# Optimization experiments

Measured on AMD Instinct MI355X. Metric: run time of the kernel, lower is better.

Reference implementation:

```python
import jax, jax.numpy as jnp
import numpy as np

N_NODES = 100000
N_EDGES = 3200000
IN_DIM, HID_DIM, N_CLASS = 64, 32, 20


def setup_inputs() -> dict:
    key = jax.random.key(0)
    k1, k2, k3, k4, k5, k6 = jax.random.split(key, 6)
    x = jax.random.normal(k1, (N_NODES, IN_DIM), dtype=jnp.float32)
    edge_index = jax.random.randint(k2, (2, N_EDGES), 0, N_NODES, dtype=jnp.int64)
    W1 = jax.random.normal(k3, (IN_DIM, HID_DIM), dtype=jnp.float32) / np.sqrt(IN_DIM)
    b1 = jnp.zeros((HID_DIM,), dtype=jnp.float32)
    Wout = jax.random.normal(k4, (HID_DIM, N_CLASS), dtype=jnp.float32) / np.sqrt(HID_DIM)
    bout = jnp.zeros((N_CLASS,), dtype=jnp.float32)
    return {"x": x, "edge_index": edge_index, "W1": W1, "b1": b1, "Wout": Wout, "bout": bout}


def gcn_conv(x, edge_index, W, b):
    # PyG GCNConv defaults: add self-loops, symmetric deg^{-1/2} normalization.
    n = x.shape[0]
    loop = jnp.arange(n, dtype=edge_index.dtype)
    row = jnp.concatenate([edge_index[0], loop])  # source
    col = jnp.concatenate([edge_index[1], loop])  # target
    deg = jax.ops.segment_sum(jnp.ones_like(col, dtype=x.dtype), col, num_segments=n)
    dis = jnp.where(deg > 0, deg ** -0.5, 0.0)
    norm = dis[row] * dis[col]  # [E+N]
    xw = x @ W  # [N, HID]
    msg = norm[:, None] * xw[row]  # [E+N, HID]
    agg = jax.ops.segment_sum(msg, col, num_segments=n)
    return agg + b


def reference(x, edge_index, W1, b1, Wout, bout):
    h = gcn_conv(x, edge_index, W1, b1)
    emb = jax.nn.relu(h)
    return emb @ Wout + bout
```

## Files before the change

kernel.cpp:

```cpp
#include <hip/hip_runtime.h>
#include <hip/hip_fp16.h>
#include <math.h>

#define N_NODES 100000
#define N_EDGES 3200000
#define IN_DIM 64
#define HID_DIM 32
#define N_CLASS 20

#define BKT_BITS 6
#define BKT_W    64
#define NBKT     1563
#define CAP_BKT  2560
#define ENT_R    (CAP_BKT / 512)

#define SUP_SHIFT 12
#define NS       25
#define CAP_S    132000
#define CH1      2048
#define NBLK1    ((N_EDGES + CH1 - 1) / CH1)
#define CH2      4096
#define BPS      ((CAP_S + CH2 - 1) / CH2)

__global__ void k_detect(const int* __restrict__ ei32, int* __restrict__ flag,
                         int* __restrict__ scursor, int* __restrict__ gcursor) {
    __shared__ int any;
    if (threadIdx.x == 0) any = 0;
    __syncthreads();
    int nz = 0;
    for (int k = threadIdx.x; k < 4096; k += blockDim.x)
        if (ei32[2 * k + 1] != 0) nz = 1;
    if (nz) atomicOr(&any, 1);
    for (int i = threadIdx.x; i < NBKT; i += blockDim.x) gcursor[i] = i * CAP_BKT;
    if (threadIdx.x < NS) scursor[threadIdx.x] = threadIdx.x * CAP_S;
    __syncthreads();
    if (threadIdx.x == 0) *flag = any ? 0 : 1;
}

__device__ __forceinline__ int get_idx(const int* __restrict__ ei32, int wide, int pos) {
    return wide ? ei32[2 * (long long)pos] : ei32[pos];
}

__global__ void __launch_bounds__(512, 4)
kS1(const int* __restrict__ ei32, const int* __restrict__ flag,
    int* __restrict__ scursor, unsigned int* __restrict__ sp) {
    __shared__ int lh[NS], lgb[NS], lrt[NS];
    int wide = *flag;
    if (threadIdx.x < NS) { lh[threadIdx.x] = 0; lrt[threadIdx.x] = 0; }
    __syncthreads();
    int base = blockIdx.x * CH1;
    int src[4], dst[4];
#pragma unroll
    for (int k = 0; k < 4; ++k) {
        int e = base + k * 512 + (int)threadIdx.x;
        if (e < N_EDGES) {
            src[k] = get_idx(ei32, wide, e);
            dst[k] = get_idx(ei32, wide, N_EDGES + e);
            atomicAdd(&lh[dst[k] >> SUP_SHIFT], 1);
        } else dst[k] = -1;
    }
    __syncthreads();
    if (threadIdx.x < NS && lh[threadIdx.x])
        lgb[threadIdx.x] = atomicAdd(&scursor[threadIdx.x], lh[threadIdx.x]);
    __syncthreads();
#pragma unroll
    for (int k = 0; k < 4; ++k) {
        if (dst[k] >= 0) {
            int s = dst[k] >> SUP_SHIFT;
            int r = atomicAdd(&lrt[s], 1);
            int pos = lgb[s] + r;
            if (pos < (s + 1) * CAP_S)
                sp[pos] = ((unsigned)src[k] << SUP_SHIFT) |
                          (unsigned)(dst[k] & ((1 << SUP_SHIFT) - 1));
        }
    }
}

__global__ void __launch_bounds__(512, 4)
kS2(const unsigned int* __restrict__ sp, const int* __restrict__ scursor,
    int* __restrict__ gcursor, unsigned int* __restrict__ pk) {
    __shared__ int lh[BKT_W], lgb[BKT_W], lrt[BKT_W];
    int s = blockIdx.x / BPS;
    int j = blockIdx.x % BPS;
    int sbase = s * CAP_S;
    int scount = min(scursor[s] - sbase, CAP_S);
    int start = j * CH2;
    if (start >= scount) return;
    int end = min(start + CH2, scount);
    if (threadIdx.x < BKT_W) { lh[threadIdx.x] = 0; lrt[threadIdx.x] = 0; }
    __syncthreads();
    unsigned ent[8]; int fb[8];
#pragma unroll
    for (int k = 0; k < 8; ++k) {
        int i = start + k * 512 + (int)threadIdx.x;
        if (i < end) {
            ent[k] = sp[sbase + i];
            fb[k] = (int)((ent[k] & ((1u << SUP_SHIFT) - 1)) >> BKT_BITS);
            atomicAdd(&lh[fb[k]], 1);
        } else fb[k] = -1;
    }
    __syncthreads();
    if (threadIdx.x < BKT_W && lh[threadIdx.x]) {
        int b = s * BKT_W + (int)threadIdx.x;
        if (b < NBKT) lgb[threadIdx.x] = atomicAdd(&gcursor[b], lh[threadIdx.x]);
    }
    __syncthreads();
#pragma unroll
    for (int k = 0; k < 8; ++k) {
        if (fb[k] >= 0) {
            int b = s * BKT_W + fb[k];
            int r = atomicAdd(&lrt[fb[k]], 1);
            int pos = lgb[fb[k]] + r;
            if (pos < (b + 1) * CAP_BKT)
                pk[pos] = ((ent[k] >> SUP_SHIFT) << BKT_BITS) | (ent[k] & (BKT_W - 1));
        }
    }
}

__global__ void kC1_deg(const unsigned int* __restrict__ pk, const int* __restrict__ gcursor,
                        float* __restrict__ dis) {
    __shared__ int lcnt[BKT_W];
    int b = blockIdx.x;
    int gb = b * CAP_BKT;
    int bsz = min(gcursor[b] - gb, CAP_BKT);
    if (threadIdx.x < BKT_W) lcnt[threadIdx.x] = 0;
    __syncthreads();
    for (int i = threadIdx.x; i < bsz; i += blockDim.x)
        atomicAdd(&lcnt[pk[gb + i] & (BKT_W - 1)], 1);
    __syncthreads();
    int node = b * BKT_W + threadIdx.x;
    if (threadIdx.x < BKT_W && node < N_NODES)
        dis[node] = rsqrtf((float)(lcnt[threadIdx.x] + 1));
}

__global__ void k_xw(const float* __restrict__ x, const float* __restrict__ W1,
                     const float* __restrict__ dis, __half* __restrict__ xw16) {
    __shared__ float sW[IN_DIM * HID_DIM];
    for (int i = threadIdx.x; i < IN_DIM * HID_DIM; i += blockDim.x) sW[i] = W1[i];
    __syncthreads();
    int tid = blockIdx.x * blockDim.x + threadIdx.x;
    int node = tid >> 3;
    int q = tid & 7;
    if (node >= N_NODES) return;
    const float4* xr = reinterpret_cast<const float4*>(x + (size_t)node * IN_DIM);
    float4 a = make_float4(0.f, 0.f, 0.f, 0.f);
#pragma unroll
    for (int k4 = 0; k4 < IN_DIM / 4; ++k4) {
        float4 xv = xr[k4];
        const float4 w0 = *reinterpret_cast<const float4*>(&sW[(k4 * 4 + 0) * HID_DIM + q * 4]);
        const float4 w1 = *reinterpret_cast<const float4*>(&sW[(k4 * 4 + 1) * HID_DIM + q * 4]);
        const float4 w2 = *reinterpret_cast<const float4*>(&sW[(k4 * 4 + 2) * HID_DIM + q * 4]);
        const float4 w3 = *reinterpret_cast<const float4*>(&sW[(k4 * 4 + 3) * HID_DIM + q * 4]);
        a.x += xv.x * w0.x + xv.y * w1.x + xv.z * w2.x + xv.w * w3.x;
        a.y += xv.x * w0.y + xv.y * w1.y + xv.z * w2.y + xv.w * w3.y;
        a.z += xv.x * w0.z + xv.y * w1.z + xv.z * w2.z + xv.w * w3.z;
        a.w += xv.x * w0.w + xv.y * w1.w + xv.z * w2.w + xv.w * w3.w;
    }
    float d = dis[node];
    union { __half2 h2[2]; uint2 u; } cvt;
    cvt.h2[0] = __floats2half2_rn(a.x * d, a.y * d);
    cvt.h2[1] = __floats2half2_rn(a.z * d, a.w * d);
    *reinterpret_cast<uint2*>(xw16 + (size_t)node * HID_DIM + q * 4) = cvt.u;
}

__device__ __forceinline__ void acc_row(float4& acc, uint2 u) {
    union U { unsigned u; __half2 hh; };
    U a0; a0.u = u.x; U a1; a1.u = u.y;
    float2 f0 = __half22float2(a0.hh);
    float2 f1 = __half22float2(a1.hh);
    acc.x += f0.x; acc.y += f0.y; acc.z += f1.x; acc.w += f1.y;
}

__global__ void __launch_bounds__(512, 8)
kD_gather(const unsigned int* __restrict__ pk, const int* __restrict__ gcursor,
          const float* __restrict__ dis, const __half* __restrict__ xw16,
          const float* __restrict__ b1, const float* __restrict__ Wout,
          const float* __restrict__ bout, float* __restrict__ out) {
    __shared__ int   ssrc[CAP_BKT];
    __shared__ int   lcnt[BKT_W], lstart[BKT_W], lrt[BKT_W];
    __shared__ float sW[HID_DIM * N_CLASS];
    __shared__ float sb1[HID_DIM];
    __shared__ float sbo[N_CLASS];
    for (int i = threadIdx.x; i < HID_DIM * N_CLASS; i += blockDim.x) sW[i] = Wout[i];
    if (threadIdx.x < HID_DIM) sb1[threadIdx.x] = b1[threadIdx.x];
    if (threadIdx.x < N_CLASS) sbo[threadIdx.x] = bout[threadIdx.x];
    if (threadIdx.x < BKT_W) { lcnt[threadIdx.x] = 0; lrt[threadIdx.x] = 0; }
    int b = blockIdx.x;
    int gb = b * CAP_BKT;
    int bsz = min(gcursor[b] - gb, CAP_BKT);
    __syncthreads();

    unsigned ents[ENT_R];
#pragma unroll
    for (int i = 0; i < ENT_R; ++i) {
        int idx = i * 512 + (int)threadIdx.x;
        ents[i] = (idx < bsz) ? pk[gb + idx] : 0xFFFFFFFFu;
    }
#pragma unroll
    for (int i = 0; i < ENT_R; ++i)
        if (ents[i] != 0xFFFFFFFFu) atomicAdd(&lcnt[ents[i] & (BKT_W - 1)], 1);
    __syncthreads();
    if (threadIdx.x < BKT_W) {
        int v = lcnt[threadIdx.x];
        int s = v;
#pragma unroll
        for (int d = 1; d < BKT_W; d <<= 1) {
            int t = __shfl_up(s, d, BKT_W);
            if ((int)threadIdx.x >= d) s += t;
        }
        lstart[threadIdx.x] = s - v;
    }
    __syncthreads();
#pragma unroll
    for (int i = 0; i < ENT_R; ++i) {
        if (ents[i] != 0xFFFFFFFFu) {
            int ld = (int)(ents[i] & (BKT_W - 1));
            int r = atomicAdd(&lrt[ld], 1);
            ssrc[lstart[ld] + r] = (int)(ents[i] >> BKT_BITS);
        }
    }
    __syncthreads();

    int grp = threadIdx.x >> 3, part = threadIdx.x & 7;
    int node = b * BKT_W + grp;
    if (node >= N_NODES) return;

    float4 acc = make_float4(0.f, 0.f, 0.f, 0.f);
    acc_row(acc, *reinterpret_cast<const uint2*>(xw16 + (size_t)node * HID_DIM + part * 4));
    float dc = dis[node];

    {
        int e = lstart[grp], end = lstart[grp] + lcnt[grp];
        while (e + 16 <= end) {
            uint2 us[16];
#pragma unroll
            for (int j = 0; j < 16; ++j) {
                int src = ssrc[e + j];
                us[j] = *reinterpret_cast<const uint2*>(xw16 + (size_t)src * HID_DIM + part * 4);
            }
#pragma unroll
            for (int j = 0; j < 16; ++j) acc_row(acc, us[j]);
            e += 16;
        }
        while (e + 4 <= end) {
            uint2 us[4];
#pragma unroll
            for (int j = 0; j < 4; ++j) {
                int src = ssrc[e + j];
                us[j] = *reinterpret_cast<const uint2*>(xw16 + (size_t)src * HID_DIM + part * 4);
            }
#pragma unroll
            for (int j = 0; j < 4; ++j) acc_row(acc, us[j]);
            e += 4;
        }
        for (; e < end; ++e) {
            int src = ssrc[e];
            acc_row(acc, *reinterpret_cast<const uint2*>(xw16 + (size_t)src * HID_DIM + part * 4));
        }
    }
    float e0 = fmaxf(dc * acc.x + sb1[part * 4 + 0], 0.f);
    float e1 = fmaxf(dc * acc.y + sb1[part * 4 + 1], 0.f);
    float e2 = fmaxf(dc * acc.z + sb1[part * 4 + 2], 0.f);
    float e3 = fmaxf(dc * acc.w + sb1[part * 4 + 3], 0.f);
    float o[N_CLASS];
#pragma unroll
    for (int cl = 0; cl < N_CLASS; ++cl) {
        o[cl] = e0 * sW[(part * 4 + 0) * N_CLASS + cl]
              + e1 * sW[(part * 4 + 1) * N_CLASS + cl]
              + e2 * sW[(part * 4 + 2) * N_CLASS + cl]
              + e3 * sW[(part * 4 + 3) * N_CLASS + cl];
    }
#pragma unroll
    for (int m = 1; m < 8; m <<= 1) {
#pragma unroll
        for (int cl = 0; cl < N_CLASS; ++cl) o[cl] += __shfl_xor(o[cl], m, 64);
    }
    if (part < 5) {
        float4 w = make_float4(o[part * 4 + 0] + sbo[part * 4 + 0],
                               o[part * 4 + 1] + sbo[part * 4 + 1],
                               o[part * 4 + 2] + sbo[part * 4 + 2],
                               o[part * 4 + 3] + sbo[part * 4 + 3]);
        *reinterpret_cast<float4*>(out + (size_t)node * N_CLASS + part * 4) = w;
    }
}

extern "C" void kernel_launch(void* const* d_in, const int* in_sizes, int n_in,
                              void* d_out, int out_size, void* d_ws, size_t ws_size,
                              hipStream_t stream) {
    const float* x    = (const float*)d_in[0];
    const int*   ei32 = (const int*)d_in[1];
    const float* W1   = (const float*)d_in[2];
    const float* b1   = (const float*)d_in[3];
    const float* Wout = (const float*)d_in[4];
    const float* bout = (const float*)d_in[5];
    float* out = (float*)d_out;

    unsigned int* sp      = (unsigned int*)d_ws;
    __half*       xw16    = (__half*)d_ws;
    unsigned int* pk      = sp + (size_t)NS * CAP_S;
    int*          gcursor = (int*)(pk + (size_t)NBKT * CAP_BKT);
    int*          scursor = gcursor + NBKT;
    float*        dis     = (float*)(scursor + NS);
    int*          flag    = (int*)(dis + N_NODES);

    k_detect<<<1, 256, 0, stream>>>(ei32, flag, scursor, gcursor);
    kS1<<<NBLK1, 512, 0, stream>>>(ei32, flag, scursor, sp);
    kS2<<<NS * BPS, 512, 0, stream>>>(sp, scursor, gcursor, pk);
    kC1_deg<<<NBKT, 256, 0, stream>>>(pk, gcursor, dis);
    k_xw<<<(N_NODES * 8 + 255) / 256, 256, 0, stream>>>(x, W1, dis, xw16);
    kD_gather<<<NBKT, 512, 0, stream>>>(pk, gcursor, dis, xw16, b1, Wout, bout, out);
}
```

Measured before the change: 123.0 us.

## Split hidden-dim gather into two feature-slice passes for cache locality

The fp16 xw table is split into two 16-wide halves stored in separate arrays. The gather kernel runs twice, once per half, so each pass's random-access working set is half the size and more likely to stay cache-resident. The second pass accumulates its partial output projection into the result written by the first. In exchange, the edge-bucket sort and local scatter are repeated in both passes, the output is read and written twice, and block size and unroll depth are reduced.

New measurement: 126.0 us. +2.4%, slower.

```diff
diff --git a/kernel.cpp b/kernel.cpp
--- a/kernel.cpp
+++ b/kernel.cpp
@@ -7,12 +7,13 @@
 #define IN_DIM 64
 #define HID_DIM 32
 #define N_CLASS 20
+#define SLICE 16
 
 #define BKT_BITS 6
 #define BKT_W    64
 #define NBKT     1563
 #define CAP_BKT  2560
-#define ENT_R    (CAP_BKT / 512)
+#define ENT_R    (CAP_BKT / 256)
 
 #define SUP_SHIFT 12
 #define NS       25
@@ -134,7 +135,8 @@
 }
 
 __global__ void k_xw(const float* __restrict__ x, const float* __restrict__ W1,
-                     const float* __restrict__ dis, __half* __restrict__ xw16) {
+                     const float* __restrict__ dis, __half* __restrict__ xwA,
+                     __half* __restrict__ xwB) {
     __shared__ float sW[IN_DIM * HID_DIM];
     for (int i = threadIdx.x; i < IN_DIM * HID_DIM; i += blockDim.x) sW[i] = W1[i];
     __syncthreads();
@@ -160,7 +162,9 @@
     union { __half2 h2[2]; uint2 u; } cvt;
     cvt.h2[0] = __floats2half2_rn(a.x * d, a.y * d);
     cvt.h2[1] = __floats2half2_rn(a.z * d, a.w * d);
-    *reinterpret_cast<uint2*>(xw16 + (size_t)node * HID_DIM + q * 4) = cvt.u;
+    __half* dst = (q < 4) ? (xwA + (size_t)node * SLICE + q * 4)
+                          : (xwB + (size_t)node * SLICE + (q - 4) * 4);
+    *reinterpret_cast<uint2*>(dst) = cvt.u;
 }
 
 __device__ __forceinline__ void acc_row(float4& acc, uint2 u) {
@@ -171,18 +175,19 @@
     acc.x += f0.x; acc.y += f0.y; acc.z += f1.x; acc.w += f1.y;
 }
 
-__global__ void __launch_bounds__(512, 8)
-kD_gather(const unsigned int* __restrict__ pk, const int* __restrict__ gcursor,
-          const float* __restrict__ dis, const __half* __restrict__ xw16,
-          const float* __restrict__ b1, const float* __restrict__ Wout,
-          const float* __restrict__ bout, float* __restrict__ out) {
+__global__ void __launch_bounds__(256, 6)
+kD_pass(const unsigned int* __restrict__ pk, const int* __restrict__ gcursor,
+        const float* __restrict__ dis, const __half* __restrict__ xws,
+        const float* __restrict__ b1, const float* __restrict__ Wout,
+        const float* __restrict__ bout, float* __restrict__ out, int P) {
     __shared__ int   ssrc[CAP_BKT];
     __shared__ int   lcnt[BKT_W], lstart[BKT_W], lrt[BKT_W];
-    __shared__ float sW[HID_DIM * N_CLASS];
-    __shared__ float sb1[HID_DIM];
+    __shared__ float sW[SLICE * N_CLASS];
+    __shared__ float sb1[SLICE];
     __shared__ float sbo[N_CLASS];
-    for (int i = threadIdx.x; i < HID_DIM * N_CLASS; i += blockDim.x) sW[i] = Wout[i];
-    if (threadIdx.x < HID_DIM) sb1[threadIdx.x] = b1[threadIdx.x];
+    for (int i = threadIdx.x; i < SLICE * N_CLASS; i += blockDim.x)
+        sW[i] = Wout[P * SLICE * N_CLASS + i];
+    if (threadIdx.x < SLICE) sb1[threadIdx.x] = b1[P * SLICE + threadIdx.x];
     if (threadIdx.x < N_CLASS) sbo[threadIdx.x] = bout[threadIdx.x];
     if (threadIdx.x < BKT_W) { lcnt[threadIdx.x] = 0; lrt[threadIdx.x] = 0; }
     int b = blockIdx.x;
@@ -193,8 +198,8 @@
     unsigned ents[ENT_R];
 #pragma unroll
     for (int i = 0; i < ENT_R; ++i) {
-        int idx = i * 512 + (int)threadIdx.x;
-        ents[i] = (idx < bsz) ? pk[gb + idx] : 0xFFFFFFFFu;
+        int idx = i * 256 + (int)threadIdx.x;
+        ents[i] = (idx < bsz) ? __builtin_nontemporal_load(pk + gb + idx) : 0xFFFFFFFFu;
     }
 #pragma unroll
     for (int i = 0; i < ENT_R; ++i)
@@ -221,42 +226,27 @@
     }
     __syncthreads();
 
-    int grp = threadIdx.x >> 3, part = threadIdx.x & 7;
+    int grp = threadIdx.x >> 2, part = threadIdx.x & 3;
     int node = b * BKT_W + grp;
     if (node >= N_NODES) return;
 
     float4 acc = make_float4(0.f, 0.f, 0.f, 0.f);
-    acc_row(acc, *reinterpret_cast<const uint2*>(xw16 + (size_t)node * HID_DIM + part * 4));
+    acc_row(acc, *reinterpret_cast<const uint2*>(xws + node * SLICE + part * 4));
     float dc = dis[node];
 
     {
         int e = lstart[grp], end = lstart[grp] + lcnt[grp];
-        while (e + 16 <= end) {
-            uint2 us[16];
-#pragma unroll
-            for (int j = 0; j < 16; ++j) {
-                int src = ssrc[e + j];
-                us[j] = *reinterpret_cast<const uint2*>(xw16 + (size_t)src * HID_DIM + part * 4);
-            }
-#pragma unroll
-            for (int j = 0; j < 16; ++j) acc_row(acc, us[j]);
-            e += 16;
-        }
-        while (e + 4 <= end) {
-            uint2 us[4];
-#pragma unroll
-            for (int j = 0; j < 4; ++j) {
-                int src = ssrc[e + j];
-                us[j] = *reinterpret_cast<const uint2*>(xw16 + (size_t)src * HID_DIM + part * 4);
-            }
-#pragma unroll
-            for (int j = 0; j < 4; ++j) acc_row(acc, us[j]);
-            e += 4;
-        }
-        for (; e < end; ++e) {
-            int src = ssrc[e];
-            acc_row(acc, *reinterpret_cast<const uint2*>(xw16 + (size_t)src * HID_DIM + part * 4));
-        }
+        while (e + 8 <= end) {
+            uint2 us[8];
+#pragma unroll
+            for (int j = 0; j < 8; ++j)
+                us[j] = *reinterpret_cast<const uint2*>(xws + ssrc[e + j] * SLICE + part * 4);
+#pragma unroll
+            for (int j = 0; j < 8; ++j) acc_row(acc, us[j]);
+            e += 8;
+        }
+        for (; e < end; ++e)
+            acc_row(acc, *reinterpret_cast<const uint2*>(xws + ssrc[e] * SLICE + part * 4));
     }
     float e0 = fmaxf(dc * acc.x + sb1[part * 4 + 0], 0.f);
     float e1 = fmaxf(dc * acc.y + sb1[part * 4 + 1], 0.f);
@@ -271,16 +261,17 @@
               + e3 * sW[(part * 4 + 3) * N_CLASS + cl];
     }
 #pragma unroll
-    for (int m = 1; m < 8; m <<= 1) {
-#pragma unroll
-        for (int cl = 0; cl < N_CLASS; ++cl) o[cl] += __shfl_xor(o[cl], m, 64);
-    }
-    if (part < 5) {
-        float4 w = make_float4(o[part * 4 + 0] + sbo[part * 4 + 0],
-                               o[part * 4 + 1] + sbo[part * 4 + 1],
-                               o[part * 4 + 2] + sbo[part * 4 + 2],
-                               o[part * 4 + 3] + sbo[part * 4 + 3]);
-        *reinterpret_cast<float4*>(out + (size_t)node * N_CLASS + part * 4) = w;
+    for (int m = 1; m < 4; m <<= 1) {
+#pragma unroll
+        for (int cl = 0; cl < N_CLASS; ++cl) o[cl] += __shfl_xor(o[cl], m, 4);
+    }
+    float* op = out + (size_t)node * N_CLASS + part * 5;
+    if (P == 0) {
+#pragma unroll
+        for (int k = 0; k < 5; ++k) op[k] = o[part * 5 + k] + sbo[part * 5 + k];
+    } else {
+#pragma unroll
+        for (int k = 0; k < 5; ++k) op[k] += o[part * 5 + k];
     }
 }
 
@@ -296,7 +287,8 @@
     float* out = (float*)d_out;
 
     unsigned int* sp      = (unsigned int*)d_ws;
-    __half*       xw16    = (__half*)d_ws;
+    __half*       xwA     = (__half*)d_ws;
+    __half*       xwB     = xwA + (size_t)N_NODES * SLICE;
     unsigned int* pk      = sp + (size_t)NS * CAP_S;
     int*          gcursor = (int*)(pk + (size_t)NBKT * CAP_BKT);
     int*          scursor = gcursor + NBKT;
@@ -307,6 +299,7 @@
     kS1<<<NBLK1, 512, 0, stream>>>(ei32, flag, scursor, sp);
     kS2<<<NS * BPS, 512, 0, stream>>>(sp, scursor, gcursor, pk);
     kC1_deg<<<NBKT, 256, 0, stream>>>(pk, gcursor, dis);
-    k_xw<<<(N_NODES * 8 + 255) / 256, 256, 0, stream>>>(x, W1, dis, xw16);
-    kD_gather<<<NBKT, 512, 0, stream>>>(pk, gcursor, dis, xw16, b1, Wout, bout, out);
-}
+    k_xw<<<(N_NODES * 8 + 255) / 256, 256, 0, stream>>>(x, W1, dis, xwA, xwB);
+    kD_pass<<<NBKT, 256, 0, stream>>>(pk, gcursor, dis, xwA, b1, Wout, bout, out, 0);
+    kD_pass<<<NBKT, 256, 0, stream>>>(pk, gcursor, dis, xwB, b1, Wout, bout, out, 1);
+}
```

## Fold degree counting into bucketing pass and drop detect and degree kernels

Applied to the files above, without the earlier changes.

Removes the separate detect kernel and degree kernel. Each kS1 block now probes its own chunk to choose between 32-bit and 64-bit indices, and cursors become relative offsets cleared by one memset. Node degrees are counted in shared memory inside kS2 and pushed to global memory with atomics, so kD_gather reads counts directly instead of re-histogramming, and the gather unroll drops from 16 to 8. The goal is fewer launches and fewer passes over the edge buckets, at the cost of a 4096-int shared histogram per kS2 block plus extra global atomics. The per-block width probe only inspects one chunk each.

Result: slower. 128.1 us (+4.1%).

```diff
diff --git a/kernel.cpp b/kernel.cpp
--- a/kernel.cpp
+++ b/kernel.cpp
@@ -15,6 +15,7 @@
 #define ENT_R    (CAP_BKT / 512)
 
 #define SUP_SHIFT 12
+#define SUP_W    (1 << SUP_SHIFT)
 #define NS       25
 #define CAP_S    132000
 #define CH1      2048
@@ -22,33 +23,24 @@
 #define CH2      4096
 #define BPS      ((CAP_S + CH2 - 1) / CH2)
 
-__global__ void k_detect(const int* __restrict__ ei32, int* __restrict__ flag,
-                         int* __restrict__ scursor, int* __restrict__ gcursor) {
-    __shared__ int any;
-    if (threadIdx.x == 0) any = 0;
-    __syncthreads();
-    int nz = 0;
-    for (int k = threadIdx.x; k < 4096; k += blockDim.x)
-        if (ei32[2 * k + 1] != 0) nz = 1;
-    if (nz) atomicOr(&any, 1);
-    for (int i = threadIdx.x; i < NBKT; i += blockDim.x) gcursor[i] = i * CAP_BKT;
-    if (threadIdx.x < NS) scursor[threadIdx.x] = threadIdx.x * CAP_S;
-    __syncthreads();
-    if (threadIdx.x == 0) *flag = any ? 0 : 1;
-}
-
 __device__ __forceinline__ int get_idx(const int* __restrict__ ei32, int wide, int pos) {
     return wide ? ei32[2 * (long long)pos] : ei32[pos];
 }
 
 __global__ void __launch_bounds__(512, 4)
-kS1(const int* __restrict__ ei32, const int* __restrict__ flag,
-    int* __restrict__ scursor, unsigned int* __restrict__ sp) {
+kS1(const int* __restrict__ ei32, int* __restrict__ scursor, unsigned int* __restrict__ sp) {
     __shared__ int lh[NS], lgb[NS], lrt[NS];
-    int wide = *flag;
+    __shared__ int sAny;
+    if (threadIdx.x == 0) sAny = 0;
     if (threadIdx.x < NS) { lh[threadIdx.x] = 0; lrt[threadIdx.x] = 0; }
-    __syncthreads();
     int base = blockIdx.x * CH1;
+    int e0 = base + (int)threadIdx.x;
+    int probe = (e0 < N_EDGES) ? ei32[2 * (long long)e0 + 1] : 0;
+    __syncthreads();
+    if (probe) sAny = 1;
+    __syncthreads();
+    int wide = (sAny == 0);
+
     int src[4], dst[4];
 #pragma unroll
     for (int k = 0; k < 4; ++k) {
@@ -68,25 +60,27 @@
         if (dst[k] >= 0) {
             int s = dst[k] >> SUP_SHIFT;
             int r = atomicAdd(&lrt[s], 1);
-            int pos = lgb[s] + r;
-            if (pos < (s + 1) * CAP_S)
-                sp[pos] = ((unsigned)src[k] << SUP_SHIFT) |
-                          (unsigned)(dst[k] & ((1 << SUP_SHIFT) - 1));
+            int rel = lgb[s] + r;
+            if (rel < CAP_S)
+                sp[(size_t)s * CAP_S + rel] = ((unsigned)src[k] << SUP_SHIFT) |
+                                              (unsigned)(dst[k] & (SUP_W - 1));
         }
     }
 }
 
 __global__ void __launch_bounds__(512, 4)
 kS2(const unsigned int* __restrict__ sp, const int* __restrict__ scursor,
-    int* __restrict__ gcursor, unsigned int* __restrict__ pk) {
+    int* __restrict__ gcursor, unsigned int* __restrict__ pk, int* __restrict__ deg) {
     __shared__ int lh[BKT_W], lgb[BKT_W], lrt[BKT_W];
+    __shared__ int ndeg[SUP_W];
     int s = blockIdx.x / BPS;
     int j = blockIdx.x % BPS;
     int sbase = s * CAP_S;
-    int scount = min(scursor[s] - sbase, CAP_S);
+    int scount = min(scursor[s], CAP_S);
     int start = j * CH2;
     if (start >= scount) return;
     int end = min(start + CH2, scount);
+    for (int i = threadIdx.x; i < SUP_W; i += 512) ndeg[i] = 0;
     if (threadIdx.x < BKT_W) { lh[threadIdx.x] = 0; lrt[threadIdx.x] = 0; }
     __syncthreads();
     unsigned ent[8]; int fb[8];
@@ -95,8 +89,10 @@
         int i = start + k * 512 + (int)threadIdx.x;
         if (i < end) {
             ent[k] = sp[sbase + i];
-            fb[k] = (int)((ent[k] & ((1u << SUP_SHIFT) - 1)) >> BKT_BITS);
+            int ld = (int)(ent[k] & (SUP_W - 1));
+            fb[k] = ld >> BKT_BITS;
             atomicAdd(&lh[fb[k]], 1);
+            atomicAdd(&ndeg[ld], 1);
         } else fb[k] = -1;
     }
     __syncthreads();
@@ -110,31 +106,22 @@
         if (fb[k] >= 0) {
             int b = s * BKT_W + fb[k];
             int r = atomicAdd(&lrt[fb[k]], 1);
-            int pos = lgb[fb[k]] + r;
-            if (pos < (b + 1) * CAP_BKT)
-                pk[pos] = ((ent[k] >> SUP_SHIFT) << BKT_BITS) | (ent[k] & (BKT_W - 1));
-        }
-    }
-}
-
-__global__ void kC1_deg(const unsigned int* __restrict__ pk, const int* __restrict__ gcursor,
-                        float* __restrict__ dis) {
-    __shared__ int lcnt[BKT_W];
-    int b = blockIdx.x;
-    int gb = b * CAP_BKT;
-    int bsz = min(gcursor[b] - gb, CAP_BKT);
-    if (threadIdx.x < BKT_W) lcnt[threadIdx.x] = 0;
-    __syncthreads();
-    for (int i = threadIdx.x; i < bsz; i += blockDim.x)
-        atomicAdd(&lcnt[pk[gb + i] & (BKT_W - 1)], 1);
-    __syncthreads();
-    int node = b * BKT_W + threadIdx.x;
-    if (threadIdx.x < BKT_W && node < N_NODES)
-        dis[node] = rsqrtf((float)(lcnt[threadIdx.x] + 1));
+            int rel = lgb[fb[k]] + r;
+            if (rel < CAP_BKT)
+                pk[(size_t)b * CAP_BKT + rel] =
+                    ((ent[k] >> SUP_SHIFT) << BKT_BITS) | (ent[k] & (BKT_W - 1));
+        }
+    }
+    __syncthreads();
+    int nodebase = s << SUP_SHIFT;
+    for (int i = threadIdx.x; i < SUP_W; i += 512) {
+        int c = ndeg[i];
+        if (c && nodebase + i < N_NODES) atomicAdd(&deg[nodebase + i], c);
+    }
 }
 
 __global__ void k_xw(const float* __restrict__ x, const float* __restrict__ W1,
-                     const float* __restrict__ dis, __half* __restrict__ xw16) {
+                     const int* __restrict__ deg, __half* __restrict__ xw16) {
     __shared__ float sW[IN_DIM * HID_DIM];
     for (int i = threadIdx.x; i < IN_DIM * HID_DIM; i += blockDim.x) sW[i] = W1[i];
     __syncthreads();
@@ -156,7 +143,7 @@
         a.z += xv.x * w0.z + xv.y * w1.z + xv.z * w2.z + xv.w * w3.z;
         a.w += xv.x * w0.w + xv.y * w1.w + xv.z * w2.w + xv.w * w3.w;
     }
-    float d = dis[node];
+    float d = rsqrtf((float)(deg[node] + 1));
     union { __half2 h2[2]; uint2 u; } cvt;
     cvt.h2[0] = __floats2half2_rn(a.x * d, a.y * d);
     cvt.h2[1] = __floats2half2_rn(a.z * d, a.w * d);
@@ -173,7 +160,7 @@
 
 __global__ void __launch_bounds__(512, 8)
 kD_gather(const unsigned int* __restrict__ pk, const int* __restrict__ gcursor,
-          const float* __restrict__ dis, const __half* __restrict__ xw16,
+          const int* __restrict__ deg, const __half* __restrict__ xw16,
           const float* __restrict__ b1, const float* __restrict__ Wout,
           const float* __restrict__ bout, float* __restrict__ out) {
     __shared__ int   ssrc[CAP_BKT];
@@ -184,39 +171,36 @@
     for (int i = threadIdx.x; i < HID_DIM * N_CLASS; i += blockDim.x) sW[i] = Wout[i];
     if (threadIdx.x < HID_DIM) sb1[threadIdx.x] = b1[threadIdx.x];
     if (threadIdx.x < N_CLASS) sbo[threadIdx.x] = bout[threadIdx.x];
-    if (threadIdx.x < BKT_W) { lcnt[threadIdx.x] = 0; lrt[threadIdx.x] = 0; }
+    if (threadIdx.x < BKT_W) lrt[threadIdx.x] = 0;
     int b = blockIdx.x;
-    int gb = b * CAP_BKT;
-    int bsz = min(gcursor[b] - gb, CAP_BKT);
-    __syncthreads();
-
+    size_t gb = (size_t)b * CAP_BKT;
+    int bsz = min(gcursor[b], CAP_BKT);
+    if (threadIdx.x < BKT_W) {
+        int node = b * BKT_W + (int)threadIdx.x;
+        int v = (node < N_NODES) ? deg[node] : 0;
+        lcnt[threadIdx.x] = v;
+        int s = v;
+#pragma unroll
+        for (int d = 1; d < BKT_W; d <<= 1) {
+            int t = __shfl_up(s, d, BKT_W);
+            if ((int)threadIdx.x >= d) s += t;
+        }
+        lstart[threadIdx.x] = s - v;
+    }
+    __syncthreads();
     unsigned ents[ENT_R];
 #pragma unroll
     for (int i = 0; i < ENT_R; ++i) {
         int idx = i * 512 + (int)threadIdx.x;
         ents[i] = (idx < bsz) ? pk[gb + idx] : 0xFFFFFFFFu;
     }
-#pragma unroll
-    for (int i = 0; i < ENT_R; ++i)
-        if (ents[i] != 0xFFFFFFFFu) atomicAdd(&lcnt[ents[i] & (BKT_W - 1)], 1);
-    __syncthreads();
-    if (threadIdx.x < BKT_W) {
-        int v = lcnt[threadIdx.x];
-        int s = v;
-#pragma unroll
-        for (int d = 1; d < BKT_W; d <<= 1) {
-            int t = __shfl_up(s, d, BKT_W);
-            if ((int)threadIdx.x >= d) s += t;
-        }
-        lstart[threadIdx.x] = s - v;
-    }
-    __syncthreads();
 #pragma unroll
     for (int i = 0; i < ENT_R; ++i) {
         if (ents[i] != 0xFFFFFFFFu) {
             int ld = (int)(ents[i] & (BKT_W - 1));
             int r = atomicAdd(&lrt[ld], 1);
-            ssrc[lstart[ld] + r] = (int)(ents[i] >> BKT_BITS);
+            int pos = lstart[ld] + r;
+            if (pos < CAP_BKT) ssrc[pos] = (int)(ents[i] >> BKT_BITS);
         }
     }
     __syncthreads();
@@ -227,36 +211,21 @@
 
     float4 acc = make_float4(0.f, 0.f, 0.f, 0.f);
     acc_row(acc, *reinterpret_cast<const uint2*>(xw16 + (size_t)node * HID_DIM + part * 4));
-    float dc = dis[node];
+    float dc = rsqrtf((float)(lcnt[grp] + 1));
 
     {
-        int e = lstart[grp], end = lstart[grp] + lcnt[grp];
-        while (e + 16 <= end) {
-            uint2 us[16];
-#pragma unroll
-            for (int j = 0; j < 16; ++j) {
-                int src = ssrc[e + j];
-                us[j] = *reinterpret_cast<const uint2*>(xw16 + (size_t)src * HID_DIM + part * 4);
-            }
-#pragma unroll
-            for (int j = 0; j < 16; ++j) acc_row(acc, us[j]);
-            e += 16;
-        }
-        while (e + 4 <= end) {
-            uint2 us[4];
-#pragma unroll
-            for (int j = 0; j < 4; ++j) {
-                int src = ssrc[e + j];
-                us[j] = *reinterpret_cast<const uint2*>(xw16 + (size_t)src * HID_DIM + part * 4);
-            }
-#pragma unroll
-            for (int j = 0; j < 4; ++j) acc_row(acc, us[j]);
-            e += 4;
-        }
-        for (; e < end; ++e) {
-            int src = ssrc[e];
-            acc_row(acc, *reinterpret_cast<const uint2*>(xw16 + (size_t)src * HID_DIM + part * 4));
-        }
+        int e = lstart[grp], end = min(lstart[grp] + lcnt[grp], CAP_BKT);
+        while (e + 8 <= end) {
+            uint2 us[8];
+#pragma unroll
+            for (int j = 0; j < 8; ++j)
+                us[j] = *reinterpret_cast<const uint2*>(xw16 + (size_t)ssrc[e + j] * HID_DIM + part * 4);
+#pragma unroll
+            for (int j = 0; j < 8; ++j) acc_row(acc, us[j]);
+            e += 8;
+        }
+        for (; e < end; ++e)
+            acc_row(acc, *reinterpret_cast<const uint2*>(xw16 + (size_t)ssrc[e] * HID_DIM + part * 4));
     }
     float e0 = fmaxf(dc * acc.x + sb1[part * 4 + 0], 0.f);
     float e1 = fmaxf(dc * acc.y + sb1[part * 4 + 1], 0.f);
@@ -300,13 +269,12 @@
     unsigned int* pk      = sp + (size_t)NS * CAP_S;
     int*          gcursor = (int*)(pk + (size_t)NBKT * CAP_BKT);
     int*          scursor = gcursor + NBKT;
-    float*        dis     = (float*)(scursor + NS);
-    int*          flag    = (int*)(dis + N_NODES);
-
-    k_detect<<<1, 256, 0, stream>>>(ei32, flag, scursor, gcursor);
-    kS1<<<NBLK1, 512, 0, stream>>>(ei32, flag, scursor, sp);
-    kS2<<<NS * BPS, 512, 0, stream>>>(sp, scursor, gcursor, pk);
-    kC1_deg<<<NBKT, 256, 0, stream>>>(pk, gcursor, dis);
-    k_xw<<<(N_NODES * 8 + 255) / 256, 256, 0, stream>>>(x, W1, dis, xw16);
-    kD_gather<<<NBKT, 512, 0, stream>>>(pk, gcursor, dis, xw16, b1, Wout, bout, out);
-}
+    int*          deg     = scursor + NS;
+
+    hipMemsetAsync(gcursor, 0, (size_t)(NBKT + NS + N_NODES) * sizeof(int), stream);
+
+    kS1<<<NBLK1, 512, 0, stream>>>(ei32, scursor, sp);
+    kS2<<<NS * BPS, 512, 0, stream>>>(sp, scursor, gcursor, pk, deg);
+    k_xw<<<(N_NODES * 8 + 255) / 256, 256, 0, stream>>>(x, W1, deg, xw16);
+    kD_gather<<<NBKT, 512, 0, stream>>>(pk, gcursor, deg, xw16, b1, Wout, bout, out);
+}
```
